# Kernel optimization log

Hardware: AMD Instinct MI355X
Metric: run time of the kernel (lower is better)

## Reference

```python
import jax, jax.numpy as jnp
import numpy as np
import math

L_, E_, H_, F_ = 6, 256, 8, 2048
NQ, B_, M_ = 300, 8, 1024

def _lin(x, w, b):
    return x @ w.T + b

def _ln(x, w, b):
    m = jnp.mean(x, -1, keepdims=True)
    v = jnp.var(x, -1, keepdims=True)
    return (x - m) / jnp.sqrt(v + 1e-5) * w + b

def _mha(q, k, v, iw, ib, ow, ob, H):
    # torch nn.MultiheadAttention, seq-first [L, B, E], packed in_proj
    E = q.shape[-1]; Dh = E // H
    wq, wk, wv = iw[:E], iw[E:2*E], iw[2*E:]
    bq, bk, bv = ib[:E], ib[E:2*E], ib[2*E:]
    qp = (_lin(q, wq, bq) * (Dh ** -0.5)).reshape(q.shape[0], q.shape[1], H, Dh)
    kp = _lin(k, wk, bk).reshape(k.shape[0], k.shape[1], H, Dh)
    vp = _lin(v, wv, bv).reshape(v.shape[0], v.shape[1], H, Dh)
    att = jax.nn.softmax(jnp.einsum('qbhd,kbhd->bhqk', qp, kp), axis=-1)
    o = jnp.einsum('bhqk,kbhd->qbhd', att, vp).reshape(q.shape[0], q.shape[1], E)
    return _lin(o, ow, ob)

def _sine4(pt):
    # pt: [nq, b, 4]; faithful to gen_sineembed_for_position4 incl. the
    # pos_w/pos_h re-use of the already-transformed pos_x/pos_y (original bug).
    dim_t = 10000.0 ** (2 * (jnp.arange(64) // 2).astype(jnp.float32) / 64)
    s = 2 * math.pi
    def iv(p):
        return jnp.stack([jnp.sin(p[:, :, 0::2]), jnp.cos(p[:, :, 1::2])], axis=3).reshape(p.shape[0], p.shape[1], -1)
    px = iv(pt[:, :, 0, None] * s / dim_t)
    py = iv(pt[:, :, 1, None] * s / dim_t)
    pw = iv(px)
    ph = iv(py)
    return jnp.concatenate([py, px, pw, ph], axis=2)


def setup_inputs() -> dict:
    key = jax.random.key(0)
    ks = iter(jax.random.split(key, 80))
    rn = lambda *s: jax.random.normal(next(ks), s, dtype=jnp.float32)
    rw = lambda *s: jax.random.normal(next(ks), s, dtype=jnp.float32) * 0.02
    d = dict(
        tgt=rn(NQ, B_, E_), memory=rn(M_, B_, E_), pos=rn(M_, B_, E_),
        query_pos=rn(NQ, B_, E_), box_embed=rn(NQ, B_, 4),
        sa_in_w=rw(L_, 3*E_, E_), sa_in_b=rw(L_, 3*E_), sa_out_w=rw(L_, E_, E_), sa_out_b=rw(L_, E_),
        ca_in_w=rw(L_, 3*E_, E_), ca_in_b=rw(L_, 3*E_), ca_out_w=rw(L_, E_, E_), ca_out_b=rw(L_, E_),
        ca_qpos_w=rw(E_, E_), ca_qpos_b=rw(E_),
        ca_kpos_w=rw(L_, E_, E_), ca_kpos_b=rw(L_, E_),
        ca_v_w=rw(L_, E_, E_), ca_v_b=rw(L_, E_),
        ca_kc_w=rw(L_, E_, E_), ca_kc_b=rw(L_, E_),
        ca_qs_w=rw(L_, E_, E_), ca_qs_b=rw(L_, E_),
        ca_vp_w=rw(L_, E_, E_), ca_vp_b=rw(L_, E_),
        lin1_w=rw(L_, F_, E_), lin1_b=rw(L_, F_), lin2_w=rw(L_, E_, F_), lin2_b=rw(L_, E_),
        lp1_w=rw(L_, F_, E_), lp1_b=rw(L_, F_), lp2_w=rw(L_, E_, F_), lp2_b=rw(L_, E_),
        norms_w=jnp.ones((L_, 6, E_), jnp.float32), norms_b=jnp.zeros((L_, 6, E_), jnp.float32),
        qs_w1=rw(E_, E_), qs_b1=rw(E_), qs_w2=rw(E_, E_), qs_b2=rw(E_),
        rh_w1=rw(E_, E_), rh_b1=rw(E_), rh_w2=rw(4, E_), rh_b2=rw(4),
        bo_w1=rw(L_, E_ // 2, 4), bo_b1=rw(L_, E_ // 2), bo_w2=rw(L_, 4, E_ // 2), bo_b2=rw(L_, 4),
    )
    return d


def _fwd(tgt, memory, pos, query_pos, box_embed, sa_in_w, sa_in_b, sa_out_w, sa_out_b,
         ca_in_w, ca_in_b, ca_out_w, ca_out_b, ca_qpos_w, ca_qpos_b, ca_kpos_w, ca_kpos_b,
         ca_v_w, ca_v_b, ca_kc_w, ca_kc_b, ca_qs_w, ca_qs_b, ca_vp_w, ca_vp_b,
         lin1_w, lin1_b, lin2_w, lin2_b, lp1_w, lp1_b, lp2_w, lp2_b, norms_w, norms_b,
         qs_w1, qs_b1, qs_w2, qs_b2, rh_w1, rh_b1, rh_w2, rh_b2, bo_w1, bo_b1, bo_w2, bo_b2):
    H = H_
    L = sa_in_w.shape[0]
    relu = jax.nn.relu
    # ref_point_head: MLP(d, d, 4, 2)
    rbs = _lin(relu(_lin(query_pos, rh_w1, rh_b1)), rh_w2, rh_b2)  # [nq,b,4]
    out = tgt
    for l in range(L):
        pt = 1.0 if l == 0 else _lin(relu(_lin(out, qs_w1, qs_b1)), qs_w2, qs_b2)
        rbs = rbs + _lin(relu(_lin(box_embed, bo_w1[l], bo_b1[l])), bo_w2[l], bo_b2[l])
        qse = _sine4(jax.nn.sigmoid(rbs)) * pt  # [nq,b,256]
        # self-attention (q = k = out + query_pos, v = out)
        q = out + query_pos
        t = _ln(out + _mha(q, q, out, sa_in_w[l], sa_in_b[l], sa_out_w[l], sa_out_b[l], H),
                norms_w[l, 0], norms_b[l, 0])
        # conditional cross-attention projections
        if l == 0:
            qc = t + _lin(query_pos, ca_qpos_w, ca_qpos_b)
            kk = memory + pos; v = memory; kpos = pos
        else:
            qc = t
            kpos = _lin(pos, ca_kpos_w[l], ca_kpos_b[l])
            v = _lin(memory, ca_v_w[l], ca_v_b[l])
            kk = _lin(memory, ca_kc_w[l], ca_kc_b[l])
        qse_p = _lin(qse, ca_qs_w[l], ca_qs_b[l])
        t2 = _mha(qc, kk, v, ca_in_w[l], ca_in_b[l], ca_out_w[l], ca_out_b[l], H)
        vpos = _lin(memory, ca_vp_w[l], ca_vp_b[l])
        t2p = _mha(qse_p, kpos, vpos, ca_in_w[l], ca_in_b[l], ca_out_w[l], ca_out_b[l], H)
        t2 = t2 + t2p
        # positional branch FFN
        tp = _ln(t + t2p, norms_w[l, 3], norms_b[l, 3])
        tp = _ln(tp + _lin(relu(_lin(tp, lp1_w[l], lp1_b[l])), lp2_w[l], lp2_b[l]),
                 norms_w[l, 4], norms_b[l, 4])
        # main branch FFN
        t = _ln(t + t2, norms_w[l, 1], norms_b[l, 1])
        t = _ln(t + _lin(relu(_lin(t, lin1_w[l], lin1_b[l])), lin2_w[l], lin2_b[l]),
                norms_w[l, 2], norms_b[l, 2])
        out = _ln(t + tp, norms_w[l, 5], norms_b[l, 5])
    return out[None]  # [1, nq, b, d] (return_intermediate=False -> unsqueeze(0))


def reference(tgt, memory, pos, query_pos, box_embed, sa_in_w, sa_in_b, sa_out_w, sa_out_b,
              ca_in_w, ca_in_b, ca_out_w, ca_out_b, ca_qpos_w, ca_qpos_b, ca_kpos_w, ca_kpos_b,
              ca_v_w, ca_v_b, ca_kc_w, ca_kc_b, ca_qs_w, ca_qs_b, ca_vp_w, ca_vp_b,
              lin1_w, lin1_b, lin2_w, lin2_b, lp1_w, lp1_b, lp2_w, lp2_b, norms_w, norms_b,
              qs_w1, qs_b1, qs_w2, qs_b2, rh_w1, rh_b1, rh_w2, rh_b2, bo_w1, bo_b1, bo_w2, bo_b2):
    return _fwd(tgt, memory, pos, query_pos, box_embed, sa_in_w, sa_in_b, sa_out_w, sa_out_b,
                ca_in_w, ca_in_b, ca_out_w, ca_out_b, ca_qpos_w, ca_qpos_b, ca_kpos_w, ca_kpos_b,
                ca_v_w, ca_v_b, ca_kc_w, ca_kc_b, ca_qs_w, ca_qs_b, ca_vp_w, ca_vp_b,
                lin1_w, lin1_b, lin2_w, lin2_b, lp1_w, lp1_b, lp2_w, lp2_b, norms_w, norms_b,
                qs_w1, qs_b1, qs_w2, qs_b2, rh_w1, rh_b1, rh_w2, rh_b2, bo_w1, bo_b1, bo_w2, bo_b2)
```

## Files before the change

kernel.cpp:

```cpp
#include <hip/hip_runtime.h>
#include <hip/hip_bf16.h>

#define NQq 300
#define BBb 8
#define MMm 1024
#define EEe 256
#define FFf 2048
#define LLl 6
#define RQ 2400
#define RM 8192
#define RPAD 2432

typedef unsigned short u16;
typedef short bf16x8 __attribute__((ext_vector_type(8)));
typedef float f32x4 __attribute__((ext_vector_type(4)));

__device__ __forceinline__ float u2f(u16 u){ return __uint_as_float(((unsigned)u)<<16); }
__device__ __forceinline__ u16 f2u(float v){
  __hip_bfloat16 h = __float2bfloat16(v);
  return *reinterpret_cast<u16*>(&h);
}
__device__ __forceinline__ int effdt(int t, int f){ return (t==0) ? 1 : ((t==1) ? 0 : (f?1:0)); }
__device__ __forceinline__ float ldd(const void* p, size_t i, int t, int f){
  if (t == 0) return ((const float*)p)[i];
  if (t == 1) return u2f(((const u16*)p)[i]);
  return f ? ((const float*)p)[i] : u2f(((const u16*)p)[i]);
}
__device__ __forceinline__ void ld8f(const void* p, size_t eoff, int e, float* o){
  if (e == 0) {
    uint4 v = *(const uint4*)((const u16*)p + eoff);
    u16 tmp[8]; *(uint4*)tmp = v;
#pragma unroll
    for (int u = 0; u < 8; ++u) o[u] = u2f(tmp[u]);
  } else {
    const float* q = (const float*)p + eoff;
    float4 v0 = ((const float4*)q)[0], v1 = ((const float4*)q)[1];
    o[0]=v0.x;o[1]=v0.y;o[2]=v0.z;o[3]=v0.w;o[4]=v1.x;o[5]=v1.y;o[6]=v1.z;o[7]=v1.w;
  }
}
__device__ __forceinline__ uint4 ld8pack(const void* p, size_t eoff, int e){
  if (e == 0) return *(const uint4*)((const u16*)p + eoff);
  float o[8]; ld8f(p, eoff, 1, o);
  u16 tmp[8];
#pragma unroll
  for (int u = 0; u < 8; ++u) tmp[u] = f2u(o[u]);
  return *(uint4*)tmp;
}

__global__ void k_flag_init(int* flag){ if (threadIdx.x==0 && blockIdx.x==0) *flag = 0; }
__global__ void k_detect(const u16* __restrict__ p, int n, int* flag){
  int hit = 0;
  for (int i = blockIdx.x*blockDim.x + threadIdx.x; i < n; i += gridDim.x*blockDim.x){
    u16 u = p[i];
    if ((u & 0x7F80u) == 0x7F80u) hit = 1;
  }
  if (hit) atomicOr(flag, 1);
}

__global__ void k_cvt_in(const void* __restrict__ s, float* __restrict__ d, int n,
                         const int* __restrict__ flag){
  int f = *flag;
  for (int i = blockIdx.x*blockDim.x + threadIdx.x; i < n; i += gridDim.x*blockDim.x)
    d[i] = ldd(s, i, 2, f);
}
__global__ void k_out_dual(const float* __restrict__ s, void* __restrict__ d, int n,
                           const int* __restrict__ flag){
  int f = *flag;
  for (int i = blockIdx.x*blockDim.x + threadIdx.x; i < n; i += gridDim.x*blockDim.x){
    if (f) ((float*)d)[i] = s[i];
    else   ((u16*)d)[i] = f2u(s[i]);
  }
}
__global__ void k_sum4(const float* __restrict__ P, size_t s, float* __restrict__ Y, int n4){
  for (int i = blockIdx.x*blockDim.x + threadIdx.x; i < n4; i += gridDim.x*blockDim.x){
    float4 a = ((const float4*)P)[i];
    float4 b = ((const float4*)(P + s))[i];
    float4 c = ((const float4*)(P + 2*s))[i];
    float4 d = ((const float4*)(P + 3*s))[i];
    float4 o; o.x=a.x+b.x+c.x+d.x; o.y=a.y+b.y+c.y+d.y;
    o.z=a.z+b.z+c.z+d.z; o.w=a.w+b.w+c.w+d.w;
    ((float4*)Y)[i] = o;
  }
}

struct CompW { const void* A[27]; size_t ao[27]; const void* B[27]; size_t bo[27]; u16* W[27]; };
__global__ __launch_bounds__(256) void k_compose_w(CompW cw, const int* __restrict__ flag){
  int f = *flag;
  int z = blockIdx.z;
  const void* A = cw.A[z]; size_t ao = cw.ao[z];
  const void* B = cw.B[z]; size_t bo = cw.bo[z];
  u16* Wo = cw.W[z];
  int ea = effdt(2,f), eb = ea;
  __shared__ __align__(16) u16 As[64*40];
  __shared__ __align__(16) u16 Bs[64*40];
  int bm = blockIdx.x*64, bn = blockIdx.y*64;
  int t = threadIdx.x;
  int lane = t & 63, wv = t >> 6;
  int wrow = (wv>>1)<<5, wcol = (wv&1)<<5;
  int quad = lane>>4, mr = lane&15;
  f32x4 a00 = {0.f,0.f,0.f,0.f}, a01 = a00, a10 = a00, a11 = a00;
  for (int k0 = 0; k0 < 256; k0 += 32){
    { int srow = t>>2, scg = (t&3)<<3;
      *(uint4*)&As[srow*40+scg] = ld8pack(A, ao + (size_t)(bm+srow)*256 + k0 + scg, ea); }
    { int kk = t>>3, c8 = (t&7)<<3;
      float o8[8]; ld8f(B, bo + (size_t)(k0+kk)*256 + bn + c8, eb, o8);
#pragma unroll
      for (int u = 0; u < 8; ++u) Bs[(c8+u)*40 + kk] = f2u(o8[u]); }
    __syncthreads();
    bf16x8 a0 = *(const bf16x8*)&As[(wrow+mr)*40+quad*8];
    bf16x8 a1 = *(const bf16x8*)&As[(wrow+16+mr)*40+quad*8];
    bf16x8 b0 = *(const bf16x8*)&Bs[(wcol+mr)*40+quad*8];
    bf16x8 b1 = *(const bf16x8*)&Bs[(wcol+16+mr)*40+quad*8];
    a00 = __builtin_amdgcn_mfma_f32_16x16x32_bf16(a0,b0,a00,0,0,0);
    a01 = __builtin_amdgcn_mfma_f32_16x16x32_bf16(a0,b1,a01,0,0,0);
    a10 = __builtin_amdgcn_mfma_f32_16x16x32_bf16(a1,b0,a10,0,0,0);
    a11 = __builtin_amdgcn_mfma_f32_16x16x32_bf16(a1,b1,a11,0,0,0);
    __syncthreads();
  }
  f32x4 av[4] = {a00,a01,a10,a11};
#pragma unroll
  for (int i = 0; i < 2; ++i)
#pragma unroll
  for (int j = 0; j < 2; ++j){
    f32x4 a = av[i*2+j];
    int col = bn + wcol + j*16 + mr;
#pragma unroll
    for (int r = 0; r < 4; ++r){
      int row = bm + wrow + i*16 + quad*4 + r;
      Wo[(size_t)row*256 + col] = f2u(a[r]);
    }
  }
}
struct CompB { const void* A[27]; size_t ao[27]; const void* b1[27]; size_t b1o[27];
               const void* b2[27]; size_t b2o[27]; u16* bo[27]; };
__global__ __launch_bounds__(256) void k_compose_b(CompB cb, const int* __restrict__ flag){
  int f = *flag;
  int z = blockIdx.x, o = threadIdx.x;
  float acc = 0.f;
  for (int j = 0; j < 256; ++j)
    acc += ldd(cb.A[z], cb.ao[z] + (size_t)o*256 + j, 2, f) * ldd(cb.b1[z], cb.b1o[z] + j, 2, f);
  cb.bo[z][o] = f2u(acc + ldd(cb.b2[z], cb.b2o[z] + o, 2, f));
}

__global__ __launch_bounds__(256) void k_gemm(
    const void* __restrict__ X1, size_t xo1, int xt1,
    const void* __restrict__ X2, size_t xo2, int xt2,
    const void* __restrict__ W1, size_t wo1, int wt1,
    const void* __restrict__ B1v, size_t bo1, int bt1,
    const void* __restrict__ W2, size_t wo2, int wt2,
    const void* __restrict__ B2v, size_t bo2, int bt2,
    void* __restrict__ Y, int yt, int ldy, size_t zstride,
    int R, int K, int O, int Rsplit, int relu, int kchunk,
    const int* __restrict__ flag)
{
  __shared__ __align__(16) u16 As[64*72];
  __shared__ __align__(16) u16 Bs[64*72];
  int f = *flag;
  int bm = blockIdx.x*64, bn = blockIdx.y*64;
  int z = blockIdx.z;
  int kbeg = z * kchunk;
  int kend = kbeg + kchunk; if (kend > K) kend = K;
  bool second = (bm >= Rsplit);
  const void* W = second ? W2 : W1;  size_t wo = second ? wo2 : wo1;  int wt = second ? wt2 : wt1;
  const void* Bv = second ? B2v : B1v; size_t bo = second ? bo2 : bo1; int bt = second ? bt2 : bt1;
  int ex1 = effdt(xt1, f), ew = effdt(wt, f);
  int t = threadIdx.x;
  int srow = t >> 2, scg = (t & 3) << 3;
  int lane = t & 63, wv = t >> 6;
  int wrow = (wv >> 1) << 5, wcol = (wv & 1) << 5;
  int quad = lane >> 4, mr = lane & 15;
  f32x4 acc00 = {0.f,0.f,0.f,0.f}, acc01 = acc00, acc10 = acc00, acc11 = acc00;
  for (int k0 = kbeg; k0 < kend; k0 += 64) {
    {
      int gr = bm + srow;
      uint4 v0 = {0u,0u,0u,0u}, v1 = v0;
      if (gr < R) {
        size_t e = xo1 + (size_t)gr*K + k0 + scg;
        if (xt2 < 0) {
          v0 = ld8pack(X1, e, ex1);
          v1 = ld8pack(X1, e + 32, ex1);
        } else {
          int ex2 = effdt(xt2, f);
          size_t e2 = xo2 + (size_t)gr*K + k0 + scg;
          float a8[8], b8[8]; u16 tmp[8];
          ld8f(X1, e, ex1, a8); ld8f(X2, e2, ex2, b8);
#pragma unroll
          for (int u = 0; u < 8; ++u) tmp[u] = f2u(a8[u] + b8[u]);
          v0 = *(uint4*)tmp;
          ld8f(X1, e + 32, ex1, a8); ld8f(X2, e2 + 32, ex2, b8);
#pragma unroll
          for (int u = 0; u < 8; ++u) tmp[u] = f2u(a8[u] + b8[u]);
          v1 = *(uint4*)tmp;
        }
      }
      *(uint4*)&As[srow*72 + scg]      = v0;
      *(uint4*)&As[srow*72 + 32 + scg] = v1;
    }
    {
      int go = bn + srow;
      uint4 v0 = {0u,0u,0u,0u}, v1 = v0;
      if (go < O) {
        size_t e = wo + (size_t)go*K + k0 + scg;
        v0 = ld8pack(W, e, ew);
        v1 = ld8pack(W, e + 32, ew);
      }
      *(uint4*)&Bs[srow*72 + scg]      = v0;
      *(uint4*)&Bs[srow*72 + 32 + scg] = v1;
    }
    __syncthreads();
#pragma unroll
    for (int ks = 0; ks < 2; ++ks) {
      int kb = ks*32 + quad*8;
      bf16x8 a0 = *(const bf16x8*)&As[(wrow      + mr)*72 + kb];
      bf16x8 a1 = *(const bf16x8*)&As[(wrow + 16 + mr)*72 + kb];
      bf16x8 b0 = *(const bf16x8*)&Bs[(wcol      + mr)*72 + kb];
      bf16x8 b1 = *(const bf16x8*)&Bs[(wcol + 16 + mr)*72 + kb];
      acc00 = __builtin_amdgcn_mfma_f32_16x16x32_bf16(a0, b0, acc00, 0, 0, 0);
      acc01 = __builtin_amdgcn_mfma_f32_16x16x32_bf16(a0, b1, acc01, 0, 0, 0);
      acc10 = __builtin_amdgcn_mfma_f32_16x16x32_bf16(a1, b0, acc10, 0, 0, 0);
      acc11 = __builtin_amdgcn_mfma_f32_16x16x32_bf16(a1, b1, acc11, 0, 0, 0);
    }
    __syncthreads();
  }
  float* Yf = (float*)Y + z*zstride;
  u16*   Yu = (u16*)Y + z*zstride;
  f32x4 av[4] = {acc00, acc01, acc10, acc11};
#pragma unroll
  for (int i = 0; i < 2; ++i)
#pragma unroll
  for (int j = 0; j < 2; ++j) {
    f32x4 a = av[i*2 + j];
    int col = bn + wcol + j*16 + mr;
    if (col >= O) continue;
    float bv = (z == 0) ? ldd(Bv, bo + col, bt, f) : 0.f;
#pragma unroll
    for (int r = 0; r < 4; ++r) {
      int row = bm + wrow + i*16 + quad*4 + r;
      if (row >= R) continue;
      float v = a[r] + bv;
      if (relu) v = fmaxf(v, 0.f);
      if (yt == 0) Yf[(size_t)row*ldy + col] = v;
      else         Yu[(size_t)row*ldy + col] = f2u(v);
    }
  }
}

__device__ __forceinline__ float blk_sum256(float v, float* red){
  for (int off = 32; off; off >>= 1) v += __shfl_down(v, off, 64);
  int lane = threadIdx.x & 63, w = threadIdx.x >> 6;
  if (lane == 0) red[w] = v;
  __syncthreads();
  v = red[0] + red[1] + red[2] + red[3];
  __syncthreads();
  return v;
}
__device__ __forceinline__ float ln_one(float x, size_t go, size_t bo,
    const void* gb, const void* bb, int f, float* red, int i){
  float m = blk_sum256(x, red) * (1.0f/256.0f);
  float d0 = x - m;
  float var = blk_sum256(d0*d0, red) * (1.0f/256.0f);
  float r = rsqrtf(var + 1e-5f);
  return d0 * r * ldd(gb, go + i, 2, f) + ldd(bb, bo + i, 2, f);
}
__global__ __launch_bounds__(256) void k_ln(
    const float* __restrict__ A, const float* __restrict__ Bp, const float* __restrict__ Cp,
    const void* __restrict__ gb, const void* __restrict__ bb, size_t o1,
    float* __restrict__ Y, const int* __restrict__ flag)
{
  __shared__ float red[4];
  int f = *flag;
  int row = blockIdx.x, i = threadIdx.x;
  size_t idx = (size_t)row*256 + i;
  float x = A[idx];
  if (Bp) x += Bp[idx];
  if (Cp) x += Cp[idx];
  Y[idx] = ln_one(x, o1, o1, gb, bb, f, red, i);
}
__global__ __launch_bounds__(256) void k_ln_pair(
    const float* __restrict__ A1, const float* __restrict__ B1, const float* __restrict__ C1,
    size_t o1, float* __restrict__ Y1,
    const float* __restrict__ A2, const float* __restrict__ B2,
    size_t o2, float* __restrict__ Y2,
    const void* __restrict__ gb, const void* __restrict__ bb, const int* __restrict__ flag)
{
  __shared__ float red[4];
  int f = *flag;
  int row = blockIdx.x, i = threadIdx.x;
  size_t idx = (size_t)row*256 + i;
  float x1 = A1[idx] + B1[idx];
  if (C1) x1 += C1[idx];
  float x2 = A2[idx] + B2[idx];
  float y1 = ln_one(x1, o1, o1, gb, bb, f, red, i);
  float y2 = ln_one(x2, o2, o2, gb, bb, f, red, i);
  Y1[idx] = y1;
  Y2[idx] = y2;
}

struct FP {
  const u16* Q[2]; int qs[2];
  const u16* K[2]; int ks[2];
  const u16* V[2]; int vs[2];
  u16* O[2];
};
__global__ __launch_bounds__(256) void k_flash_pair(FP fp, int NQr, int Nk, float scale)
{
  __shared__ __align__(16) u16 Qs[64*40];
  __shared__ __align__(16) u16 Ks[64*40];
  __shared__ __align__(16) u16 Vs[32*72];
  __shared__ __align__(16) u16 Ps[64*72];
  int z = blockIdx.z;
  const u16* Q = fp.Q[z]; int qstr = fp.qs[z];
  const u16* K = fp.K[z]; int kstr = fp.ks[z];
  const u16* V = fp.V[z]; int vstr = fp.vs[z];
  u16* O = fp.O[z];
  int t = threadIdx.x;
  int b = blockIdx.y >> 3, h = blockIdx.y & 7;
  int q0 = blockIdx.x * 64;
  int lane = t & 63, wv = t >> 6;
  int quad = lane >> 4, mr = lane & 15;
  {
    int qi = t >> 2, c8 = (t & 3) * 8;
    int qg = q0 + qi; if (qg >= NQr) qg = NQr - 1;
    *(uint4*)&Qs[qi*40 + c8] = *(const uint4*)(Q + ((size_t)qg*8 + b)*qstr + h*32 + c8);
  }
  f32x4 o0 = {0.f,0.f,0.f,0.f}, o1 = o0;
  float m_run[4], l_run[4];
#pragma unroll
  for (int r = 0; r < 4; ++r){ m_run[r] = -1e30f; l_run[r] = 0.f; }
  __syncthreads();

  for (int k0 = 0; k0 < Nk; k0 += 64) {
    {
      int ki = t >> 2, c8 = (t & 3)*8;
      int kg = k0 + ki;
      uint4 kv = {0u,0u,0u,0u}, vv = {0u,0u,0u,0u};
      if (kg < Nk) {
        kv = *(const uint4*)(K + ((size_t)kg*8 + b)*kstr + h*32 + c8);
        vv = *(const uint4*)(V + ((size_t)kg*8 + b)*vstr + h*32 + c8);
      }
      *(uint4*)&Ks[ki*40 + c8] = kv;
      u16 tmp[8]; *(uint4*)tmp = vv;
#pragma unroll
      for (int u = 0; u < 8; ++u) Vs[(c8+u)*72 + ki] = tmp[u];
    }
    __syncthreads();
    bf16x8 aq = *(const bf16x8*)&Qs[(wv*16 + mr)*40 + quad*8];
    f32x4 s[4];
#pragma unroll
    for (int j = 0; j < 4; ++j) {
      bf16x8 bk = *(const bf16x8*)&Ks[(j*16 + mr)*40 + quad*8];
      f32x4 zz = {0.f,0.f,0.f,0.f};
      s[j] = __builtin_amdgcn_mfma_f32_16x16x32_bf16(aq, bk, zz, 0, 0, 0);
      s[j] *= scale;
    }
    float alpha[4];
#pragma unroll
    for (int r = 0; r < 4; ++r) {
      float cm = -1e30f;
#pragma unroll
      for (int j = 0; j < 4; ++j) {
        int kg = k0 + j*16 + mr;
        cm = fmaxf(cm, (kg < Nk) ? s[j][r] : -1e30f);
      }
      for (int msk = 1; msk < 16; msk <<= 1)
        cm = fmaxf(cm, __shfl_xor(cm, msk, 64));
      float mn = fmaxf(m_run[r], cm);
      alpha[r] = __expf(m_run[r] - mn);
      m_run[r] = mn;
      float rsum = 0.f;
#pragma unroll
      for (int j = 0; j < 4; ++j) {
        int kg = k0 + j*16 + mr;
        float p = (kg < Nk) ? __expf(s[j][r] - mn) : 0.f;
        s[j][r] = p;
        rsum += p;
      }
      for (int msk = 1; msk < 16; msk <<= 1)
        rsum += __shfl_xor(rsum, msk, 64);
      l_run[r] = l_run[r]*alpha[r] + rsum;
    }
#pragma unroll
    for (int j = 0; j < 4; ++j)
#pragma unroll
      for (int r = 0; r < 4; ++r)
        Ps[(wv*16 + quad*4 + r)*72 + j*16 + mr] = f2u(s[j][r]);
    __syncthreads();
    f32x4 pv0 = {0.f,0.f,0.f,0.f}, pv1 = pv0;
#pragma unroll
    for (int st = 0; st < 2; ++st) {
      bf16x8 ap  = *(const bf16x8*)&Ps[(wv*16 + mr)*72 + st*32 + quad*8];
      bf16x8 bv0 = *(const bf16x8*)&Vs[(mr)*72      + st*32 + quad*8];
      bf16x8 bv1 = *(const bf16x8*)&Vs[(16 + mr)*72 + st*32 + quad*8];
      pv0 = __builtin_amdgcn_mfma_f32_16x16x32_bf16(ap, bv0, pv0, 0, 0, 0);
      pv1 = __builtin_amdgcn_mfma_f32_16x16x32_bf16(ap, bv1, pv1, 0, 0, 0);
    }
#pragma unroll
    for (int r = 0; r < 4; ++r) {
      o0[r] = o0[r]*alpha[r] + pv0[r];
      o1[r] = o1[r]*alpha[r] + pv1[r];
    }
    __syncthreads();
  }
#pragma unroll
  for (int r = 0; r < 4; ++r) {
    int qg = q0 + wv*16 + quad*4 + r;
    if (qg >= NQr) continue;
    float inv = 1.0f / l_run[r];
    u16* dst = O + ((size_t)qg*8 + b)*256 + h*32;
    dst[mr]      = f2u(o0[r]*inv);
    dst[16 + mr] = f2u(o1[r]*inv);
  }
}

__global__ __launch_bounds__(256) void k_boxsine(
    const void* __restrict__ box, const void* __restrict__ w1, size_t w1o,
    const void* __restrict__ b1v, size_t b1o,
    const void* __restrict__ w2, size_t w2o, const void* __restrict__ b2v, size_t b2o,
    float* __restrict__ RBS, const u16* __restrict__ pt, u16* __restrict__ qse,
    const int* __restrict__ flag)
{
  int f = *flag;
  int row = blockIdx.x, t = threadIdx.x;
  __shared__ float xs[4];
  __shared__ float hs[128];
  __shared__ float rb[4];
  if (t < 4) xs[t] = ldd(box, (size_t)row*4 + t, 2, f);
  __syncthreads();
  if (t < 128) {
    float acc = ldd(b1v, b1o + t, 2, f);
#pragma unroll
    for (int j = 0; j < 4; ++j) acc += ldd(w1, w1o + (size_t)t*4 + j, 2, f) * xs[j];
    hs[t] = fmaxf(acc, 0.f);
  }
  __syncthreads();
  if (t < 4) {
    float acc = ldd(b2v, b2o + t, 2, f);
    for (int j = 0; j < 128; ++j) acc += ldd(w2, w2o + (size_t)t*128 + j, 2, f) * hs[j];
    float nr = RBS[(size_t)row*4 + t] + acc;
    RBS[(size_t)row*4 + t] = nr;
    rb[t] = nr;
  }
  __syncthreads();
  int c = t >> 6, i = t & 63;
  float x = 1.f/(1.f + __expf(-rb[0]));
  float y = 1.f/(1.f + __expf(-rb[1]));
  int j = i >> 1;
  float dt = powf(10000.f, (float)(2*j)/64.f);
  const float s2pi = 6.283185307179586f;
  float base = (c == 0 || c == 3) ? y : x;
  float a = base * s2pi / dt;
  bool even = ((i & 1) == 0);
  float p1 = even ? sinf(a) : cosf(a);
  float v = (c <= 1) ? p1 : (even ? sinf(p1) : cosf(p1));
  if (pt) v *= u2f(pt[(size_t)row*256 + t]);
  qse[(size_t)row*256 + t] = f2u(v);
}

extern "C" void kernel_launch(void* const* d_in, const int* in_sizes, int n_in,
                              void* d_out, int out_size, void* d_ws, size_t ws_size,
                              hipStream_t stream) {
  (void)in_sizes; (void)n_in; (void)out_size; (void)ws_size;

  int* FLAG = (int*)d_ws;
  float* f32p = (float*)((char*)d_ws + 16);
  size_t fo = 0;
  auto AF = [&](size_t n){ float* p = f32p + fo; fo += n; return p; };
  float* OUT = AF(614400);
  float* T   = AF((size_t)RPAD*256);
  float* TP  = AF((size_t)RPAD*256);
  float* T2  = AF(614400);
  float* T2P = AF(614400);
  float* Q1  = AF((size_t)2*RPAD*256);
  float* PART= AF((size_t)4*2*RPAD*256);
  float* RBS = AF(9600);
  u16* u16p = (u16*)(f32p + fo);
  size_t uo = 0;
  auto AU = [&](size_t n){ u16* p = u16p + uo; uo += (n + 7) & ~(size_t)7; return p; };
  u16* QSE  = AU(614400);
  u16* QC   = AU(614400);
  u16* AO   = AU(2*614400);
  u16* PT   = AU(614400);
  u16* QB   = AU(2*614400);
  u16* QKB  = AU(1228800);
  u16* KVV  = AU((size_t)RM*768);
  u16* KPOS = AU((size_t)RM*256);
  u16* KSPARE = AU((size_t)RM*256);
  u16* HID  = KVV;
  u16* SAV  = KPOS;
  u16* QPW  = AU(6*65536);  u16* QPB  = AU(6*256);
  u16* KVVW = AU(5*196608); u16* KVVB = AU(5*768);
  u16* KPW  = AU(5*65536);  u16* KPB  = AU(5*256);
  u16* VP0W = AU(65536);    u16* VP0B = AU(256);
  (void)KSPARE;

  k_flag_init<<<1,64,0,stream>>>(FLAG);
  k_detect<<<256,256,0,stream>>>((const u16*)d_in[1], 262144, FLAG);
  k_cvt_in<<<600,256,0,stream>>>(d_in[0], OUT, RQ*EEe, FLAG);

  {
    CompW cw; CompB cb; int nz = 0;
    auto addc = [&](int ia, size_t ao, int ib, size_t bo_, u16* W,
                    int ib1, size_t b1o, int ib2, size_t b2o, u16* bo){
      cw.A[nz]=d_in[ia]; cw.ao[nz]=ao; cw.B[nz]=d_in[ib]; cw.bo[nz]=bo_; cw.W[nz]=W;
      cb.A[nz]=d_in[ia]; cb.ao[nz]=ao; cb.b1[nz]=d_in[ib1]; cb.b1o[nz]=b1o;
      cb.b2[nz]=d_in[ib2]; cb.b2o[nz]=b2o; cb.bo[nz]=bo; ++nz;
    };
    for (int l = 0; l < 6; ++l)
      addc(9,(size_t)l*196608, 21,(size_t)l*65536, QPW+(size_t)l*65536,
           22,(size_t)l*256, 10,(size_t)l*768, QPB+(size_t)l*256);
    for (int l = 1; l < 6; ++l) {
      size_t wk = (size_t)l*196608 + 65536, wv = (size_t)l*196608 + 131072;
      u16* WS = KVVW + (size_t)(l-1)*196608;
      u16* BS = KVVB + (size_t)(l-1)*768;
      addc(9,wk, 19,(size_t)l*65536, WS,        20,(size_t)l*256, 10,(size_t)l*768+256, BS);
      addc(9,wv, 17,(size_t)l*65536, WS+65536,  18,(size_t)l*256, 10,(size_t)l*768+512, BS+256);
      addc(9,wv, 23,(size_t)l*65536, WS+131072, 24,(size_t)l*256, 10,(size_t)l*768+512, BS+512);
      addc(9,wk, 15,(size_t)l*65536, KPW+(size_t)(l-1)*65536,
           16,(size_t)l*256, 10,(size_t)l*768+256, KPB+(size_t)(l-1)*256);
    }
    addc(9,131072, 23,0, VP0W, 24,0, 10,512, VP0B);
    k_compose_w<<<dim3(4,4,27),256,0,stream>>>(cw, FLAG);
    k_compose_b<<<27,256,0,stream>>>(cb, FLAG);
  }

  struct P { const void* p; size_t o; int t; };
  auto GEMM = [&](P X1, P X2, P W1, P B1, P W2, P B2, void* Y, int yt, int ldy,
                  int R, int K, int O, int Rsplit, int relu, int kc, int gz, size_t zs){
    dim3 g((R+63)/64, (O+63)/64, gz);
    k_gemm<<<g,256,0,stream>>>(X1.p,X1.o,X1.t, X2.p,X2.o,X2.t, W1.p,W1.o,W1.t,
                               B1.p,B1.o,B1.t, W2.p,W2.o,W2.t, B2.p,B2.o,B2.t,
                               Y,yt,ldy,zs,R,K,O,Rsplit,relu,kc,FLAG);
  };
  P NONE = {nullptr, 0, -1};
  auto RAW = [&](int i, size_t o){ P p = {d_in[i], o, 2}; return p; };
  auto WS1 = [&](const u16* q){ P p = {q, 0, 1}; return p; };
  auto WS0 = [&](const float* q){ P p = {q, 0, 0}; return p; };
  auto G1 = [&](P X, P W, P B, void* Y, int yt, int ldy, int R, int K, int O, int relu){
    GEMM(X, NONE, W, B, W, B, Y, yt, ldy, R, K, O, R+64, relu, K, 1, 0);
  };
  auto G2 = [&](P X, P X2, P W, P B, void* Y, int yt, int ldy, int R, int K, int O){
    GEMM(X, X2, W, B, W, B, Y, yt, ldy, R, K, O, R+64, 0, K, 1, 0);
  };
  auto LN1k = [&](const float* A, const float* Bp, const float* Cp, int l, int j, float* Y){
    size_t o1 = ((size_t)l*6 + j)*EEe;
    k_ln<<<RQ,256,0,stream>>>(A,Bp,Cp, d_in[33], d_in[34], o1, Y, FLAG);
  };
  const float rs = 0.17677669529663687f;

  G1(RAW(3,0), RAW(39,0), RAW(40,0), QC, 1, 256, RQ, 256, 256, 1);
  G1(WS1(QC),  RAW(41,0), RAW(42,0), RBS, 0, 4,  RQ, 256, 4,   0);

  for (int l = 0; l < LLl; ++l) {
    size_t sw = (size_t)l*196608, sb = (size_t)l*768;
    if (l > 0) {
      G1(WS0(OUT), RAW(35,0), RAW(36,0), QC, 1, 256, RQ, 256, 256, 1);
      G1(WS1(QC),  RAW(37,0), RAW(38,0), PT, 1, 256, RQ, 256, 256, 0);
    }
    k_boxsine<<<RQ,256,0,stream>>>(d_in[4], d_in[43],(size_t)l*512, d_in[44],(size_t)l*128,
                                   d_in[45],(size_t)l*512, d_in[46],(size_t)l*4,
                                   RBS, l > 0 ? PT : (const u16*)nullptr, QSE, FLAG);

    G2(WS0(OUT), RAW(3,0), RAW(5,sw), RAW(6,sb), QKB, 1, 512, RQ, 256, 512);
    G1(WS0(OUT), RAW(5,sw+131072), RAW(6,sb+512), SAV, 1, 256, RQ, 256, 256, 0);
    {
      FP fp = {};
      fp.Q[0]=QKB; fp.qs[0]=512; fp.K[0]=QKB+256; fp.ks[0]=512;
      fp.V[0]=SAV; fp.vs[0]=256; fp.O[0]=AO;
      k_flash_pair<<<dim3(5,64,1),256,0,stream>>>(fp, NQq, NQq, rs);
    }
    G1(WS1(AO), RAW(7,(size_t)l*65536), RAW(8,(size_t)l*256), Q1, 0, 256, RQ, 256, 256, 0);
    LN1k(OUT, Q1, nullptr, l, 0, T);

    if (l == 0) {
      G2(RAW(1,0), RAW(2,0), RAW(9,sw+65536), RAW(10,sb+256), KVV, 1, 768, RM, 256, 256);
      G1(RAW(1,0), RAW(9,sw+131072), RAW(10,sb+512), KVV+256, 1, 768, RM, 256, 256, 0);
      G1(RAW(1,0), WS1(VP0W), WS1(VP0B), KVV+512, 1, 768, RM, 256, 256, 0);
      G1(RAW(2,0), RAW(9,sw+65536), RAW(10,sb+256), KPOS, 1, 256, RM, 256, 256, 0);
    } else {
      G1(RAW(1,0), WS1(KVVW+(size_t)(l-1)*196608), WS1(KVVB+(size_t)(l-1)*768),
         KVV, 1, 768, RM, 256, 768, 0);
      G1(RAW(2,0), WS1(KPW+(size_t)(l-1)*65536), WS1(KPB+(size_t)(l-1)*256),
         KPOS, 1, 256, RM, 256, 256, 0);
    }

    if (l == 0) {
      G1(RAW(3,0), RAW(13,0), RAW(14,0), Q1, 0, 256, RQ, 256, 256, 0);
      G2(WS0(T), WS0(Q1), RAW(9,sw), RAW(10,sb), QB, 1, 256, RQ, 256, 256);
    } else {
      G1(WS0(T), RAW(9,sw), RAW(10,sb), QB, 1, 256, RQ, 256, 256, 0);
    }
    G1(WS1(QSE), WS1(QPW+(size_t)l*65536), WS1(QPB+(size_t)l*256),
       QB+614400, 1, 256, RQ, 256, 256, 0);

    {
      FP fp = {};
      fp.Q[0]=QB;        fp.qs[0]=256; fp.K[0]=KVV;     fp.ks[0]=768;
      fp.V[0]=KVV+256;   fp.vs[0]=768; fp.O[0]=AO;
      fp.Q[1]=QB+614400; fp.qs[1]=256; fp.K[1]=KPOS;    fp.ks[1]=256;
      fp.V[1]=KVV+512;   fp.vs[1]=768; fp.O[1]=AO+614400;
      k_flash_pair<<<dim3(5,64,2),256,0,stream>>>(fp, NQq, MMm, rs);
    }
    G1(WS1(AO), RAW(11,(size_t)l*65536), RAW(12,(size_t)l*256),
       T2, 0, 256, 2*RQ, 256, 256, 0);

    k_ln_pair<<<RQ,256,0,stream>>>(T, T2, T2P, ((size_t)l*6+1)*EEe, T,
                                   T, T2P, ((size_t)l*6+3)*EEe, TP,
                                   d_in[33], d_in[34], FLAG);

    GEMM(WS0(T), NONE, RAW(25,(size_t)l*524288), RAW(26,(size_t)l*2048),
         RAW(29,(size_t)l*524288), RAW(30,(size_t)l*2048),
         HID, 1, 2048, 2*RPAD, 256, 2048, RPAD, 1, 256, 1, 0);
    GEMM(WS1(HID), NONE, RAW(27,(size_t)l*524288), RAW(28,(size_t)l*256),
         RAW(31,(size_t)l*524288), RAW(32,(size_t)l*256),
         PART, 0, 256, 2*RPAD, 2048, 256, RPAD, 0, 512, 4, (size_t)2*RPAD*256);
    k_sum4<<<1216,256,0,stream>>>(PART, (size_t)2*RPAD*256, Q1, (2*RPAD*256)/4);

    k_ln_pair<<<RQ,256,0,stream>>>(T, Q1, nullptr, ((size_t)l*6+2)*EEe, T,
                                   TP, Q1 + (size_t)RPAD*256, ((size_t)l*6+4)*EEe, TP,
                                   d_in[33], d_in[34], FLAG);

    LN1k(T, TP, nullptr, l, 5, OUT);
  }

  k_out_dual<<<600,256,0,stream>>>(OUT, d_out, RQ*EEe, FLAG);
}
```

Before: 2.028 ms.

## Prefetch next tiles into registers in GEMM and flash attention, and double-buffer K/V

The GEMM now loads the next K-tile of X and W into registers while MFMAs run on the current shared-memory tile. Flash attention double-buffers K/V in shared memory and prefetches the next tile into registers. It drops two of its three barriers per iteration, relying on each wave reading only its own Ps rows. It also folds log2(e) into the scale so it can use exp2f, rotates the V transpose store order to reduce bank conflicts, and swaps the grid so batch-head is the fast dimension. The cost is higher register and LDS use, which may reduce occupancy.

```diff
diff --git a/kernel.cpp b/kernel.cpp
--- a/kernel.cpp
+++ b/kernel.cpp
@@ -169,45 +169,53 @@
   int lane = t & 63, wv = t >> 6;
   int wrow = (wv >> 1) << 5, wcol = (wv & 1) << 5;
   int quad = lane >> 4, mr = lane & 15;
+  int gr = bm + srow, go = bn + srow;
+
+  uint4 xa0, xa1, wb0, wb1;
+  auto loadX = [&](int k0, uint4& v0, uint4& v1){
+    v0 = (uint4){0u,0u,0u,0u}; v1 = v0;
+    if (gr < R) {
+      size_t e = xo1 + (size_t)gr*K + k0 + scg;
+      if (xt2 < 0) {
+        v0 = ld8pack(X1, e, ex1);
+        v1 = ld8pack(X1, e + 32, ex1);
+      } else {
+        int ex2 = effdt(xt2, f);
+        size_t e2 = xo2 + (size_t)gr*K + k0 + scg;
+        float a8[8], b8[8]; u16 tmp[8];
+        ld8f(X1, e, ex1, a8); ld8f(X2, e2, ex2, b8);
+#pragma unroll
+        for (int u = 0; u < 8; ++u) tmp[u] = f2u(a8[u] + b8[u]);
+        v0 = *(uint4*)tmp;
+        ld8f(X1, e + 32, ex1, a8); ld8f(X2, e2 + 32, ex2, b8);
+#pragma unroll
+        for (int u = 0; u < 8; ++u) tmp[u] = f2u(a8[u] + b8[u]);
+        v1 = *(uint4*)tmp;
+      }
+    }
+  };
+  auto loadW = [&](int k0, uint4& v0, uint4& v1){
+    v0 = (uint4){0u,0u,0u,0u}; v1 = v0;
+    if (go < O) {
+      size_t e = wo + (size_t)go*K + k0 + scg;
+      v0 = ld8pack(W, e, ew);
+      v1 = ld8pack(W, e + 32, ew);
+    }
+  };
+  loadX(kbeg, xa0, xa1);
+  loadW(kbeg, wb0, wb1);
+
   f32x4 acc00 = {0.f,0.f,0.f,0.f}, acc01 = acc00, acc10 = acc00, acc11 = acc00;
   for (int k0 = kbeg; k0 < kend; k0 += 64) {
-    {
-      int gr = bm + srow;
-      uint4 v0 = {0u,0u,0u,0u}, v1 = v0;
-      if (gr < R) {
-        size_t e = xo1 + (size_t)gr*K + k0 + scg;
-        if (xt2 < 0) {
-          v0 = ld8pack(X1, e, ex1);
-          v1 = ld8pack(X1, e + 32, ex1);
-        } else {
-          int ex2 = effdt(xt2, f);
-          size_t e2 = xo2 + (size_t)gr*K + k0 + scg;
-          float a8[8], b8[8]; u16 tmp[8];
-          ld8f(X1, e, ex1, a8); ld8f(X2, e2, ex2, b8);
-#pragma unroll
-          for (int u = 0; u < 8; ++u) tmp[u] = f2u(a8[u] + b8[u]);
-          v0 = *(uint4*)tmp;
-          ld8f(X1, e + 32, ex1, a8); ld8f(X2, e2 + 32, ex2, b8);
-#pragma unroll
-          for (int u = 0; u < 8; ++u) tmp[u] = f2u(a8[u] + b8[u]);
-          v1 = *(uint4*)tmp;
-        }
-      }
-      *(uint4*)&As[srow*72 + scg]      = v0;
-      *(uint4*)&As[srow*72 + 32 + scg] = v1;
-    }
-    {
-      int go = bn + srow;
-      uint4 v0 = {0u,0u,0u,0u}, v1 = v0;
-      if (go < O) {
-        size_t e = wo + (size_t)go*K + k0 + scg;
-        v0 = ld8pack(W, e, ew);
-        v1 = ld8pack(W, e + 32, ew);
-      }
-      *(uint4*)&Bs[srow*72 + scg]      = v0;
-      *(uint4*)&Bs[srow*72 + 32 + scg] = v1;
-    }
+    *(uint4*)&As[srow*72 + scg]      = xa0;
+    *(uint4*)&As[srow*72 + 32 + scg] = xa1;
+    *(uint4*)&Bs[srow*72 + scg]      = wb0;
+    *(uint4*)&Bs[srow*72 + 32 + scg] = wb1;
     __syncthreads();
+    if (k0 + 64 < kend) {
+      loadX(k0 + 64, xa0, xa1);
+      loadW(k0 + 64, wb0, wb1);
+    }
 #pragma unroll
     for (int ks = 0; ks < 2; ++ks) {
       int kb = ks*32 + quad*8;
@@ -305,8 +313,8 @@
 __global__ __launch_bounds__(256) void k_flash_pair(FP fp, int NQr, int Nk, float scale)
 {
   __shared__ __align__(16) u16 Qs[64*40];
-  __shared__ __align__(16) u16 Ks[64*40];
-  __shared__ __align__(16) u16 Vs[32*72];
+  __shared__ __align__(16) u16 Ks[2][64*40];
+  __shared__ __align__(16) u16 Vs[2][32*72];
   __shared__ __align__(16) u16 Ps[64*72];
   int z = blockIdx.z;
   const u16* Q = fp.Q[z]; int qstr = fp.qs[z];
@@ -314,41 +322,52 @@
   const u16* V = fp.V[z]; int vstr = fp.vs[z];
   u16* O = fp.O[z];
   int t = threadIdx.x;
-  int b = blockIdx.y >> 3, h = blockIdx.y & 7;
-  int q0 = blockIdx.x * 64;
+  int bh = blockIdx.x;
+  int b = bh >> 3, h = bh & 7;
+  int q0 = blockIdx.y * 64;
   int lane = t & 63, wv = t >> 6;
   int quad = lane >> 4, mr = lane & 15;
+  int ki = t >> 2, c8 = (t & 3) * 8;
+  int rot = (t & 3) * 2;
   {
-    int qi = t >> 2, c8 = (t & 3) * 8;
-    int qg = q0 + qi; if (qg >= NQr) qg = NQr - 1;
-    *(uint4*)&Qs[qi*40 + c8] = *(const uint4*)(Q + ((size_t)qg*8 + b)*qstr + h*32 + c8);
+    int qg = q0 + ki; if (qg >= NQr) qg = NQr - 1;
+    *(uint4*)&Qs[ki*40 + c8] = *(const uint4*)(Q + ((size_t)qg*8 + b)*qstr + h*32 + c8);
+  }
+  uint4 kv = {0u,0u,0u,0u}, vv = kv;
+  if (ki < Nk) {
+    kv = *(const uint4*)(K + ((size_t)ki*8 + b)*kstr + h*32 + c8);
+    vv = *(const uint4*)(V + ((size_t)ki*8 + b)*vstr + h*32 + c8);
   }
   f32x4 o0 = {0.f,0.f,0.f,0.f}, o1 = o0;
   float m_run[4], l_run[4];
 #pragma unroll
   for (int r = 0; r < 4; ++r){ m_run[r] = -1e30f; l_run[r] = 0.f; }
-  __syncthreads();
 
   for (int k0 = 0; k0 < Nk; k0 += 64) {
+    int buf = (k0 >> 6) & 1;
+    *(uint4*)&Ks[buf][ki*40 + c8] = kv;
     {
-      int ki = t >> 2, c8 = (t & 3)*8;
-      int kg = k0 + ki;
-      uint4 kv = {0u,0u,0u,0u}, vv = {0u,0u,0u,0u};
+      u16 tmp[8]; *(uint4*)tmp = vv;
+#pragma unroll
+      for (int u = 0; u < 8; ++u){
+        int up = (u + rot) & 7;
+        Vs[buf][(c8+up)*72 + ki] = tmp[up];
+      }
+    }
+    if (k0 + 64 < Nk) {
+      int kg = k0 + 64 + ki;
+      kv = (uint4){0u,0u,0u,0u}; vv = kv;
       if (kg < Nk) {
         kv = *(const uint4*)(K + ((size_t)kg*8 + b)*kstr + h*32 + c8);
         vv = *(const uint4*)(V + ((size_t)kg*8 + b)*vstr + h*32 + c8);
       }
-      *(uint4*)&Ks[ki*40 + c8] = kv;
-      u16 tmp[8]; *(uint4*)tmp = vv;
-#pragma unroll
-      for (int u = 0; u < 8; ++u) Vs[(c8+u)*72 + ki] = tmp[u];
     }
     __syncthreads();
     bf16x8 aq = *(const bf16x8*)&Qs[(wv*16 + mr)*40 + quad*8];
     f32x4 s[4];
 #pragma unroll
     for (int j = 0; j < 4; ++j) {
-      bf16x8 bk = *(const bf16x8*)&Ks[(j*16 + mr)*40 + quad*8];
+      bf16x8 bk = *(const bf16x8*)&Ks[buf][(j*16 + mr)*40 + quad*8];
       f32x4 zz = {0.f,0.f,0.f,0.f};
       s[j] = __builtin_amdgcn_mfma_f32_16x16x32_bf16(aq, bk, zz, 0, 0, 0);
       s[j] *= scale;
@@ -365,13 +384,13 @@
       for (int msk = 1; msk < 16; msk <<= 1)
         cm = fmaxf(cm, __shfl_xor(cm, msk, 64));
       float mn = fmaxf(m_run[r], cm);
-      alpha[r] = __expf(m_run[r] - mn);
+      alpha[r] = exp2f(m_run[r] - mn);
       m_run[r] = mn;
       float rsum = 0.f;
 #pragma unroll
       for (int j = 0; j < 4; ++j) {
         int kg = k0 + j*16 + mr;
-        float p = (kg < Nk) ? __expf(s[j][r] - mn) : 0.f;
+        float p = (kg < Nk) ? exp2f(s[j][r] - mn) : 0.f;
         s[j][r] = p;
         rsum += p;
       }
@@ -384,13 +403,12 @@
 #pragma unroll
       for (int r = 0; r < 4; ++r)
         Ps[(wv*16 + quad*4 + r)*72 + j*16 + mr] = f2u(s[j][r]);
-    __syncthreads();
     f32x4 pv0 = {0.f,0.f,0.f,0.f}, pv1 = pv0;
 #pragma unroll
     for (int st = 0; st < 2; ++st) {
       bf16x8 ap  = *(const bf16x8*)&Ps[(wv*16 + mr)*72 + st*32 + quad*8];
-      bf16x8 bv0 = *(const bf16x8*)&Vs[(mr)*72      + st*32 + quad*8];
-      bf16x8 bv1 = *(const bf16x8*)&Vs[(16 + mr)*72 + st*32 + quad*8];
+      bf16x8 bv0 = *(const bf16x8*)&Vs[buf][(mr)*72      + st*32 + quad*8];
+      bf16x8 bv1 = *(const bf16x8*)&Vs[buf][(16 + mr)*72 + st*32 + quad*8];
       pv0 = __builtin_amdgcn_mfma_f32_16x16x32_bf16(ap, bv0, pv0, 0, 0, 0);
       pv1 = __builtin_amdgcn_mfma_f32_16x16x32_bf16(ap, bv1, pv1, 0, 0, 0);
     }
@@ -399,7 +417,6 @@
       o0[r] = o0[r]*alpha[r] + pv0[r];
       o1[r] = o1[r]*alpha[r] + pv1[r];
     }
-    __syncthreads();
   }
 #pragma unroll
   for (int r = 0; r < 4; ++r) {
@@ -545,7 +562,7 @@
     size_t o1 = ((size_t)l*6 + j)*EEe;
     k_ln<<<RQ,256,0,stream>>>(A,Bp,Cp, d_in[33], d_in[34], o1, Y, FLAG);
   };
-  const float rs = 0.17677669529663687f;
+  const float rs2 = 0.17677669529663687f * 1.4426950408889634f;
 
   G1(RAW(3,0), RAW(39,0), RAW(40,0), QC, 1, 256, RQ, 256, 256, 1);
   G1(WS1(QC),  RAW(41,0), RAW(42,0), RBS, 0, 4,  RQ, 256, 4,   0);
@@ -566,7 +583,7 @@
       FP fp = {};
       fp.Q[0]=QKB; fp.qs[0]=512; fp.K[0]=QKB+256; fp.ks[0]=512;
       fp.V[0]=SAV; fp.vs[0]=256; fp.O[0]=AO;
-      k_flash_pair<<<dim3(5,64,1),256,0,stream>>>(fp, NQq, NQq, rs);
+      k_flash_pair<<<dim3(64,5,1),256,0,stream>>>(fp, NQq, NQq, rs2);
     }
     G1(WS1(AO), RAW(7,(size_t)l*65536), RAW(8,(size_t)l*256), Q1, 0, 256, RQ, 256, 256, 0);
     LN1k(OUT, Q1, nullptr, l, 0, T);
@@ -598,7 +615,7 @@
       fp.V[0]=KVV+256;   fp.vs[0]=768; fp.O[0]=AO;
       fp.Q[1]=QB+614400; fp.qs[1]=256; fp.K[1]=KPOS;    fp.ks[1]=256;
       fp.V[1]=KVV+512;   fp.vs[1]=768; fp.O[1]=AO+614400;
-      k_flash_pair<<<dim3(5,64,2),256,0,stream>>>(fp, NQq, MMm, rs);
+      k_flash_pair<<<dim3(64,5,2),256,0,stream>>>(fp, NQq, MMm, rs2);
     }
     G1(WS1(AO), RAW(11,(size_t)l*65536), RAW(12,(size_t)l*256),
        T2, 0, 256, 2*RQ, 256, 256, 0);
```

Result: slower. 2.091 ms (+3.1%).
